# Kernel optimization log

Measured on AMD Instinct MI355X. Metric: run time of the kernel, lower is better.

Reference implementation:

```python
import jax, jax.numpy as jnp
import numpy as np

N = 50000
E = 800000
D = 128
NCLASS = 10


def setup_inputs() -> dict:
    key = jax.random.key(0)
    ks = jax.random.split(key, 12)
    stdv = 1.0 / np.sqrt(D)
    inp = {
        "x": jax.random.normal(ks[0], (N, D), dtype=jnp.float32),
        "edge_src": jax.random.randint(ks[1], (E,), 0, N, dtype=jnp.int32),
        "edge_dst": jax.random.randint(ks[2], (E,), 0, N, dtype=jnp.int32),
        "edge_weight": jax.random.uniform(ks[3], (E,), dtype=jnp.float32),
        "W1": jax.random.uniform(ks[4], (D, D), jnp.float32, -stdv, stdv),
        "b1": jax.random.uniform(ks[5], (D,), jnp.float32, -stdv, stdv),
        "W2": jax.random.uniform(ks[6], (D, D), jnp.float32, -stdv, stdv),
        "b2": jax.random.uniform(ks[7], (D,), jnp.float32, -stdv, stdv),
        "W3": jax.random.uniform(ks[8], (D, D), jnp.float32, -stdv, stdv),
        "b3": jax.random.uniform(ks[9], (D,), jnp.float32, -stdv, stdv),
        "lin_W": jax.random.normal(ks[10], (NCLASS, 3 * D), dtype=jnp.float32) * 0.05,
        "lin_b": jax.random.normal(ks[11], (NCLASS,), dtype=jnp.float32) * 0.05,
    }
    return inp


def _gcn_layer(h, W, b, edge_src, edge_dst, edge_weight):
    # support = h @ W  (dense GEMM), then spmm(adj, support) as gather-scale-scatter
    support = h @ W                                   # [N, out]
    msgs = support[edge_src] * edge_weight[:, None]   # [E, out]
    agg = jax.ops.segment_sum(msgs, edge_dst, num_segments=h.shape[0])
    return agg + b


def reference(x, edge_src, edge_dst, edge_weight, W1, b1, W2, b2, W3, b3, lin_W, lin_b):
    x1 = jax.nn.relu(_gcn_layer(x, W1, b1, edge_src, edge_dst, edge_weight))
    o1 = jnp.max(x1, axis=0)
    x2 = jax.nn.relu(_gcn_layer(x1, W2, b2, edge_src, edge_dst, edge_weight))
    o2 = jnp.max(x2, axis=0)
    x3 = _gcn_layer(x2, W3, b3, edge_src, edge_dst, edge_weight)
    o3 = jnp.max(x3, axis=0)
    lin_in = jnp.concatenate([o1, o2, o3], axis=0)    # [3*D]
    logits = lin_W @ lin_in + lin_b                   # [nclass]
    return jax.nn.log_softmax(logits, axis=0)
```

## Files before the change

kernel.cpp:

```cpp
#include <hip/hip_runtime.h>
#include <hip/hip_bf16.h>
#include <math.h>

#define NN 50000
#define NPAD 50048
#define NE 800000
#define DD 128
#define NCLS 10
#define SCAN_BLOCK 1024
#define NTILES ((NN + 1 + SCAN_BLOCK - 1) / SCAN_BLOCK)

typedef short s16x8 __attribute__((ext_vector_type(8)));
typedef float f32x4 __attribute__((ext_vector_type(4)));

__device__ __forceinline__ unsigned short f2bf(float x) {
  __hip_bfloat16 h = __float2bfloat16(x);
  return __builtin_bit_cast(unsigned short, h);
}
__device__ __forceinline__ float bflo(unsigned int u) { return __uint_as_float(u << 16); }
__device__ __forceinline__ float bfhi(unsigned int u) { return __uint_as_float(u & 0xFFFF0000u); }

__device__ __forceinline__ unsigned int fkey(float f) {
  unsigned int u = __float_as_uint(f);
  return u ^ ((u & 0x80000000u) ? 0xFFFFFFFFu : 0x80000000u);
}
__device__ __forceinline__ float funkey(unsigned int k) {
  unsigned int u = (k & 0x80000000u) ? (k ^ 0x80000000u) : ~k;
  return __uint_as_float(u);
}

__global__ void k_init(int* __restrict__ offs, unsigned int* __restrict__ omax) {
  int i = blockIdx.x * blockDim.x + threadIdx.x;
  if (i < NN + 1) offs[i] = 0;
  if (i < 3 * DD) omax[i] = 0u;
}

__global__ void k_count(const int* __restrict__ edst, int* __restrict__ offs) {
  int e = blockIdx.x * blockDim.x + threadIdx.x;
  if (e < NE) atomicAdd(&offs[edst[e] + 1], 1);
}

__global__ void k_scan_partial(const int* __restrict__ offs, int* __restrict__ bsum) {
  __shared__ int red[SCAN_BLOCK];
  int i = blockIdx.x * SCAN_BLOCK + threadIdx.x;
  red[threadIdx.x] = (i < NN + 1) ? offs[i] : 0;
  __syncthreads();
  for (int off = SCAN_BLOCK / 2; off > 0; off >>= 1) {
    if ((int)threadIdx.x < off) red[threadIdx.x] += red[threadIdx.x + off];
    __syncthreads();
  }
  if (threadIdx.x == 0) bsum[blockIdx.x] = red[0];
}

__global__ void k_scan_bsum(int* __restrict__ bsum) {
  if (threadIdx.x == 0) {
    int run = 0;
    for (int i = 0; i < NTILES; ++i) { int v = bsum[i]; bsum[i] = run; run += v; }
  }
}

__global__ void k_scan_final(int* __restrict__ offs, const int* __restrict__ bsum,
                             int* __restrict__ cursor) {
  __shared__ int tmp[SCAN_BLOCK];
  int i = blockIdx.x * SCAN_BLOCK + threadIdx.x;
  int v = (i < NN + 1) ? offs[i] : 0;
  tmp[threadIdx.x] = v;
  __syncthreads();
  for (int off = 1; off < SCAN_BLOCK; off <<= 1) {
    int t = ((int)threadIdx.x >= off) ? tmp[threadIdx.x - off] : 0;
    __syncthreads();
    tmp[threadIdx.x] += t;
    __syncthreads();
  }
  int incl = tmp[threadIdx.x] + bsum[blockIdx.x];
  if (i < NN + 1) {
    offs[i] = incl;
    if (i < NN) cursor[i] = incl;
  }
}

__global__ void k_fill(const int* __restrict__ esrc, const int* __restrict__ edst,
                       const float* __restrict__ ew, int* __restrict__ cursor,
                       int2* __restrict__ csr) {
  int e = blockIdx.x * blockDim.x + threadIdx.x;
  if (e < NE) {
    int d = edst[e];
    int p = atomicAdd(&cursor[d], 1);
    csr[p] = make_int2(esrc[e], __float_as_int(ew[e]));
  }
}

__global__ __launch_bounds__(256) void k_cvtW(const float* __restrict__ W1,
    const float* __restrict__ W2, const float* __restrict__ W3,
    unsigned short* __restrict__ WT1, unsigned short* __restrict__ WT2,
    unsigned short* __restrict__ WT3) {
  int i = blockIdx.x * 256 + threadIdx.x;
  if (i < DD * DD) {
    int k = i >> 7, c = i & 127;
    WT1[c * DD + k] = f2bf(W1[i]);
    WT2[c * DD + k] = f2bf(W2[i]);
    WT3[c * DD + k] = f2bf(W3[i]);
  }
}

template <int F32IN>
__global__ __launch_bounds__(256) void k_mm(const void* __restrict__ Hv,
                                            const unsigned short* __restrict__ Wt,
                                            unsigned short* __restrict__ S) {
  const int wave = threadIdx.x >> 6, lane = threadIdx.x & 63;
  const int gw = blockIdx.x * 4 + wave;
  const int r0 = (gw >> 1) * 32;
  const int cbase = (gw & 1) * 64;
  const int l15 = lane & 15, lk = (lane >> 4) * 8;

  s16x8 Af[4][4];
#pragma unroll
  for (int m = 0; m < 4; ++m)
#pragma unroll
    for (int ks = 0; ks < 4; ++ks)
      Af[m][ks] = *(const s16x8*)&Wt[(cbase + m * 16 + l15) * DD + ks * 32 + lk];

  s16x8 Bf[2][4];
#pragma unroll
  for (int n = 0; n < 2; ++n) {
    const int r = r0 + n * 16 + l15;
    if (F32IN) {
      const float* H = (const float*)Hv;
#pragma unroll
      for (int ks = 0; ks < 4; ++ks) {
        float4 a = make_float4(0.f, 0.f, 0.f, 0.f), b = a;
        if (r < NN) {
          a = *(const float4*)&H[(size_t)r * DD + ks * 32 + lk];
          b = *(const float4*)&H[(size_t)r * DD + ks * 32 + lk + 4];
        }
        s16x8 f;
        f[0] = (short)f2bf(a.x); f[1] = (short)f2bf(a.y);
        f[2] = (short)f2bf(a.z); f[3] = (short)f2bf(a.w);
        f[4] = (short)f2bf(b.x); f[5] = (short)f2bf(b.y);
        f[6] = (short)f2bf(b.z); f[7] = (short)f2bf(b.w);
        Bf[n][ks] = f;
      }
    } else {
      const unsigned short* H = (const unsigned short*)Hv;
#pragma unroll
      for (int ks = 0; ks < 4; ++ks)
        Bf[n][ks] = *(const s16x8*)&H[(size_t)r * DD + ks * 32 + lk];
    }
  }

  f32x4 acc[4][2];
#pragma unroll
  for (int m = 0; m < 4; ++m)
#pragma unroll
    for (int n = 0; n < 2; ++n) acc[m][n] = (f32x4){0.f, 0.f, 0.f, 0.f};

#pragma unroll
  for (int ks = 0; ks < 4; ++ks)
#pragma unroll
    for (int m = 0; m < 4; ++m)
#pragma unroll
      for (int n = 0; n < 2; ++n)
        acc[m][n] = __builtin_amdgcn_mfma_f32_16x16x32_bf16(Af[m][ks], Bf[n][ks],
                                                            acc[m][n], 0, 0, 0);

  const int csub = 4 * (lane >> 4);
#pragma unroll
  for (int m = 0; m < 4; ++m)
#pragma unroll
    for (int n = 0; n < 2; ++n) {
      uint2 pv;
      pv.x = (uint)f2bf(acc[m][n][0]) | ((uint)f2bf(acc[m][n][1]) << 16);
      pv.y = (uint)f2bf(acc[m][n][2]) | ((uint)f2bf(acc[m][n][3]) << 16);
      *(uint2*)&S[(size_t)(r0 + n * 16 + l15) * DD + cbase + m * 16 + csub] = pv;
    }
}

__device__ __forceinline__ void fma8(float* acc, float w, uint4 u) {
  acc[0] = fmaf(w, bflo(u.x), acc[0]);
  acc[1] = fmaf(w, bfhi(u.x), acc[1]);
  acc[2] = fmaf(w, bflo(u.y), acc[2]);
  acc[3] = fmaf(w, bfhi(u.y), acc[3]);
  acc[4] = fmaf(w, bflo(u.z), acc[4]);
  acc[5] = fmaf(w, bfhi(u.z), acc[5]);
  acc[6] = fmaf(w, bflo(u.w), acc[6]);
  acc[7] = fmaf(w, bfhi(u.w), acc[7]);
}

__global__ __launch_bounds__(256) void k_agg(const unsigned short* __restrict__ S,
                                             const int2* __restrict__ csr,
                                             const int* __restrict__ offs,
                                             const float* __restrict__ bias,
                                             unsigned short* __restrict__ Xout,
                                             unsigned int* __restrict__ omax,
                                             int do_relu) {
  __shared__ unsigned int cmax[DD];
  for (int i = threadIdx.x; i < DD; i += 256) cmax[i] = 0u;
  __syncthreads();
  const int lane = threadIdx.x & 63;
  const int wave = threadIdx.x >> 6;
  const int q = lane >> 4;
  const int t = lane & 15;
  const int gwave = blockIdx.x * 4 + wave;
  const int nwaves = gridDim.x * 4;

  float bcol[8];
  {
    float4 b0 = *(const float4*)&bias[t * 8];
    float4 b1 = *(const float4*)&bias[t * 8 + 4];
    bcol[0] = b0.x; bcol[1] = b0.y; bcol[2] = b0.z; bcol[3] = b0.w;
    bcol[4] = b1.x; bcol[5] = b1.y; bcol[6] = b1.z; bcol[7] = b1.w;
  }
  float mx[8];
#pragma unroll
  for (int j = 0; j < 8; ++j) mx[j] = -INFINITY;

  for (int d = gwave; d < NN; d += nwaves) {
    const int e0 = offs[d], e1 = offs[d + 1];
    float acc[8] = {0.f, 0.f, 0.f, 0.f, 0.f, 0.f, 0.f, 0.f};
    int e = e0 + q;
    const int nfull = (e1 - e0) >> 4;
    for (int s = 0; s < nfull; ++s, e += 16) {
      int2 c0 = csr[e];
      int2 c1 = csr[e + 4];
      int2 c2 = csr[e + 8];
      int2 c3 = csr[e + 12];
      uint4 u0 = *(const uint4*)&S[(size_t)c0.x * DD + t * 8];
      uint4 u1 = *(const uint4*)&S[(size_t)c1.x * DD + t * 8];
      uint4 u2 = *(const uint4*)&S[(size_t)c2.x * DD + t * 8];
      uint4 u3 = *(const uint4*)&S[(size_t)c3.x * DD + t * 8];
      fma8(acc, __int_as_float(c0.y), u0);
      fma8(acc, __int_as_float(c1.y), u1);
      fma8(acc, __int_as_float(c2.y), u2);
      fma8(acc, __int_as_float(c3.y), u3);
    }
    while (__any(e < e1)) {
      if (e < e1) {
        int2 c = csr[e];
        uint4 u = *(const uint4*)&S[(size_t)c.x * DD + t * 8];
        fma8(acc, __int_as_float(c.y), u);
      }
      e += 4;
    }
#pragma unroll
    for (int j = 0; j < 8; ++j) {
      acc[j] += __shfl_xor(acc[j], 16, 64);
      acc[j] += __shfl_xor(acc[j], 32, 64);
      acc[j] += bcol[j];
      if (do_relu) acc[j] = fmaxf(acc[j], 0.f);
      mx[j] = fmaxf(mx[j], acc[j]);
    }
    if (Xout && q == 0) {
      uint4 xv;
      xv.x = (uint)f2bf(acc[0]) | ((uint)f2bf(acc[1]) << 16);
      xv.y = (uint)f2bf(acc[2]) | ((uint)f2bf(acc[3]) << 16);
      xv.z = (uint)f2bf(acc[4]) | ((uint)f2bf(acc[5]) << 16);
      xv.w = (uint)f2bf(acc[6]) | ((uint)f2bf(acc[7]) << 16);
      *(uint4*)&Xout[(size_t)d * DD + t * 8] = xv;
    }
  }
  if (q == 0) {
#pragma unroll
    for (int j = 0; j < 8; ++j) atomicMax(&cmax[t * 8 + j], fkey(mx[j]));
  }
  __syncthreads();
  for (int i = threadIdx.x; i < DD; i += 256) atomicMax(&omax[i], cmax[i]);
}

__global__ void k_head(const unsigned int* __restrict__ omax,
                       const float* __restrict__ linW,
                       const float* __restrict__ linb,
                       float* __restrict__ out) {
  __shared__ float o[3 * DD];
  __shared__ float logits[NCLS];
  int t = threadIdx.x;
  if (t < 3 * DD) o[t] = funkey(omax[t]);
  __syncthreads();
  if (t < NCLS) {
    float acc = linb[t];
    for (int j = 0; j < 3 * DD; ++j) acc = fmaf(linW[t * 3 * DD + j], o[j], acc);
    logits[t] = acc;
  }
  __syncthreads();
  if (t == 0) {
    float m = -INFINITY;
    for (int c = 0; c < NCLS; ++c) m = fmaxf(m, logits[c]);
    float s = 0.f;
    for (int c = 0; c < NCLS; ++c) s += expf(logits[c] - m);
    float ls = logf(s);
    for (int c = 0; c < NCLS; ++c) out[c] = logits[c] - m - ls;
  }
}

extern "C" void kernel_launch(void* const* d_in, const int* in_sizes, int n_in,
                              void* d_out, int out_size, void* d_ws, size_t ws_size,
                              hipStream_t stream) {
  const float* x    = (const float*)d_in[0];
  const int*   esrc = (const int*)d_in[1];
  const int*   edst = (const int*)d_in[2];
  const float* ew   = (const float*)d_in[3];
  const float* W1   = (const float*)d_in[4];
  const float* b1   = (const float*)d_in[5];
  const float* W2   = (const float*)d_in[6];
  const float* b2   = (const float*)d_in[7];
  const float* W3   = (const float*)d_in[8];
  const float* b3   = (const float*)d_in[9];
  const float* linW = (const float*)d_in[10];
  const float* linb = (const float*)d_in[11];
  float* out = (float*)d_out;

  size_t off = 0;
  auto alloc = [&](size_t bytes) {
    void* p = (char*)d_ws + off;
    off += (bytes + 255) & ~(size_t)255;
    return p;
  };
  unsigned short* X1   = (unsigned short*)alloc((size_t)NPAD * DD * 2);
  unsigned short* X2   = (unsigned short*)alloc((size_t)NPAD * DD * 2);
  unsigned short* S    = (unsigned short*)alloc((size_t)NPAD * DD * 2);
  unsigned short* WT1  = (unsigned short*)alloc((size_t)DD * DD * 2);
  unsigned short* WT2  = (unsigned short*)alloc((size_t)DD * DD * 2);
  unsigned short* WT3  = (unsigned short*)alloc((size_t)DD * DD * 2);
  int*          offs   = (int*)alloc((NN + 1) * 4);
  int*          cursor = (int*)alloc(NN * 4);
  int2*         csr    = (int2*)alloc((size_t)NE * 8);
  unsigned int* omax   = (unsigned int*)alloc(3 * DD * 4);
  int*          bsum   = (int*)alloc(NTILES * 4);
  (void)ws_size; (void)n_in; (void)in_sizes; (void)out_size;

  k_init<<<(NN + 256) / 256, 256, 0, stream>>>(offs, omax);
  k_count<<<(NE + 255) / 256, 256, 0, stream>>>(edst, offs);
  k_scan_partial<<<NTILES, SCAN_BLOCK, 0, stream>>>(offs, bsum);
  k_scan_bsum<<<1, 64, 0, stream>>>(bsum);
  k_scan_final<<<NTILES, SCAN_BLOCK, 0, stream>>>(offs, bsum, cursor);
  k_fill<<<(NE + 255) / 256, 256, 0, stream>>>(esrc, edst, ew, cursor, csr);

  k_cvtW<<<(DD * DD + 255) / 256, 256, 0, stream>>>(W1, W2, W3, WT1, WT2, WT3);

  const int mm_grid = (NPAD / 32) * 2 / 4;
  k_mm<1><<<mm_grid, 256, 0, stream>>>(x, WT1, S);
  k_agg<<<2048, 256, 0, stream>>>(S, csr, offs, b1, X1, omax, 1);
  k_mm<0><<<mm_grid, 256, 0, stream>>>(X1, WT2, S);
  k_agg<<<2048, 256, 0, stream>>>(S, csr, offs, b2, X2, omax + DD, 1);
  k_mm<0><<<mm_grid, 256, 0, stream>>>(X2, WT3, S);
  k_agg<<<2048, 256, 0, stream>>>(S, csr, offs, b3, nullptr, omax + 2 * DD, 0);

  k_head<<<1, 384, 0, stream>>>(omax, linW, linb, out);
}
```

Baseline: 438.6 us.

## Stage GEMM row tiles in swizzled LDS and deepen aggregation gather unroll

The dense GEMM kernel now loads each 32-row input tile once into XOR-swizzled shared memory with coalesced 16-byte loads. Four waves each compute 32 output columns from that shared tile, and the result is staged back through LDS so the store to S is fully coalesced. Before, each wave loaded its own strided fragments straight from global memory. Separately, the aggregation loop is unrolled to 8 gathers in flight per lane, with a 16-edge remainder step, to expose more memory-level parallelism. The change adds barriers and LDS use per block, and the extra registers could reduce occupancy.

```diff
diff --git a/kernel.cpp b/kernel.cpp
--- a/kernel.cpp
+++ b/kernel.cpp
@@ -107,72 +107,97 @@
 __global__ __launch_bounds__(256) void k_mm(const void* __restrict__ Hv,
                                             const unsigned short* __restrict__ Wt,
                                             unsigned short* __restrict__ S) {
+  __shared__ unsigned short Hl[32 * DD];
+  char* lb = (char*)Hl;
   const int wave = threadIdx.x >> 6, lane = threadIdx.x & 63;
-  const int gw = blockIdx.x * 4 + wave;
-  const int r0 = (gw >> 1) * 32;
-  const int cbase = (gw & 1) * 64;
-  const int l15 = lane & 15, lk = (lane >> 4) * 8;
-
-  s16x8 Af[4][4];
-#pragma unroll
-  for (int m = 0; m < 4; ++m)
-#pragma unroll
-    for (int ks = 0; ks < 4; ++ks)
-      Af[m][ks] = *(const s16x8*)&Wt[(cbase + m * 16 + l15) * DD + ks * 32 + lk];
-
-  s16x8 Bf[2][4];
-#pragma unroll
-  for (int n = 0; n < 2; ++n) {
-    const int r = r0 + n * 16 + l15;
+  const int l15 = lane & 15, lk16 = (lane >> 4);
+  const int r0 = blockIdx.x * 32;
+
+#pragma unroll
+  for (int j = 0; j < 2; ++j) {
+    const int idx = threadIdx.x + j * 256;
+    const int B = idx * 16;
+    const int row = B >> 8;
+    const int addr = B ^ ((row & 7) << 4);
     if (F32IN) {
       const float* H = (const float*)Hv;
-#pragma unroll
-      for (int ks = 0; ks < 4; ++ks) {
-        float4 a = make_float4(0.f, 0.f, 0.f, 0.f), b = a;
-        if (r < NN) {
-          a = *(const float4*)&H[(size_t)r * DD + ks * 32 + lk];
-          b = *(const float4*)&H[(size_t)r * DD + ks * 32 + lk + 4];
-        }
-        s16x8 f;
-        f[0] = (short)f2bf(a.x); f[1] = (short)f2bf(a.y);
-        f[2] = (short)f2bf(a.z); f[3] = (short)f2bf(a.w);
-        f[4] = (short)f2bf(b.x); f[5] = (short)f2bf(b.y);
-        f[6] = (short)f2bf(b.z); f[7] = (short)f2bf(b.w);
-        Bf[n][ks] = f;
+      const int r = r0 + row;
+      float4 a = make_float4(0.f, 0.f, 0.f, 0.f), b = a;
+      if (r < NN) {
+        const float* src = H + (size_t)r * DD + ((B & 255) >> 1);
+        a = *(const float4*)src;
+        b = *(const float4*)(src + 4);
       }
+      uint4 pv;
+      pv.x = (uint)f2bf(a.x) | ((uint)f2bf(a.y) << 16);
+      pv.y = (uint)f2bf(a.z) | ((uint)f2bf(a.w) << 16);
+      pv.z = (uint)f2bf(b.x) | ((uint)f2bf(b.y) << 16);
+      pv.w = (uint)f2bf(b.z) | ((uint)f2bf(b.w) << 16);
+      *(uint4*)(lb + addr) = pv;
     } else {
-      const unsigned short* H = (const unsigned short*)Hv;
-#pragma unroll
-      for (int ks = 0; ks < 4; ++ks)
-        Bf[n][ks] = *(const s16x8*)&H[(size_t)r * DD + ks * 32 + lk];
-    }
-  }
-
-  f32x4 acc[4][2];
-#pragma unroll
-  for (int m = 0; m < 4; ++m)
+      const char* H = (const char*)Hv;
+      uint4 v = *(const uint4*)(H + (size_t)r0 * 256 + B);
+      *(uint4*)(lb + addr) = v;
+    }
+  }
+  __syncthreads();
+
+  const int cbase = wave * 32;
+  s16x8 Af[2][4];
+#pragma unroll
+  for (int m = 0; m < 2; ++m)
+#pragma unroll
+    for (int ks = 0; ks < 4; ++ks)
+      Af[m][ks] = *(const s16x8*)&Wt[(cbase + m * 16 + l15) * DD + ks * 32 + lk16 * 8];
+
+  s16x8 Bf[2][4];
+#pragma unroll
+  for (int n = 0; n < 2; ++n) {
+    const int row = n * 16 + l15;
+#pragma unroll
+    for (int ks = 0; ks < 4; ++ks) {
+      const int B = row * 256 + ks * 64 + lk16 * 16;
+      Bf[n][ks] = *(const s16x8*)(lb + (B ^ ((row & 7) << 4)));
+    }
+  }
+
+  f32x4 acc[2][2];
+#pragma unroll
+  for (int m = 0; m < 2; ++m)
 #pragma unroll
     for (int n = 0; n < 2; ++n) acc[m][n] = (f32x4){0.f, 0.f, 0.f, 0.f};
 
 #pragma unroll
   for (int ks = 0; ks < 4; ++ks)
 #pragma unroll
-    for (int m = 0; m < 4; ++m)
+    for (int m = 0; m < 2; ++m)
 #pragma unroll
       for (int n = 0; n < 2; ++n)
         acc[m][n] = __builtin_amdgcn_mfma_f32_16x16x32_bf16(Af[m][ks], Bf[n][ks],
                                                             acc[m][n], 0, 0, 0);
 
-  const int csub = 4 * (lane >> 4);
-#pragma unroll
-  for (int m = 0; m < 4; ++m)
+  __syncthreads();
+#pragma unroll
+  for (int m = 0; m < 2; ++m)
 #pragma unroll
     for (int n = 0; n < 2; ++n) {
+      const int row = n * 16 + l15;
+      const int colb = (cbase + m * 16 + 4 * lk16) * 2;
+      const int B = row * 256 + colb;
       uint2 pv;
       pv.x = (uint)f2bf(acc[m][n][0]) | ((uint)f2bf(acc[m][n][1]) << 16);
       pv.y = (uint)f2bf(acc[m][n][2]) | ((uint)f2bf(acc[m][n][3]) << 16);
-      *(uint2*)&S[(size_t)(r0 + n * 16 + l15) * DD + cbase + m * 16 + csub] = pv;
-    }
+      *(uint2*)(lb + (B ^ ((row & 7) << 4))) = pv;
+    }
+  __syncthreads();
+#pragma unroll
+  for (int j = 0; j < 2; ++j) {
+    const int idx = threadIdx.x + j * 256;
+    const int B = idx * 16;
+    const int row = B >> 8;
+    uint4 v = *(const uint4*)(lb + (B ^ ((row & 7) << 4)));
+    *(uint4*)((char*)S + (size_t)r0 * 256 + B) = v;
+  }
 }
 
 __device__ __forceinline__ void fma8(float* acc, float w, uint4 u) {
@@ -202,6 +227,7 @@
   const int t = lane & 15;
   const int gwave = blockIdx.x * 4 + wave;
   const int nwaves = gridDim.x * 4;
+  const unsigned short* Scol = S + t * 8;
 
   float bcol[8];
   {
@@ -216,27 +242,49 @@
 
   for (int d = gwave; d < NN; d += nwaves) {
     const int e0 = offs[d], e1 = offs[d + 1];
+    const int nedge = e1 - e0;
     float acc[8] = {0.f, 0.f, 0.f, 0.f, 0.f, 0.f, 0.f, 0.f};
     int e = e0 + q;
-    const int nfull = (e1 - e0) >> 4;
-    for (int s = 0; s < nfull; ++s, e += 16) {
-      int2 c0 = csr[e];
-      int2 c1 = csr[e + 4];
-      int2 c2 = csr[e + 8];
-      int2 c3 = csr[e + 12];
-      uint4 u0 = *(const uint4*)&S[(size_t)c0.x * DD + t * 8];
-      uint4 u1 = *(const uint4*)&S[(size_t)c1.x * DD + t * 8];
-      uint4 u2 = *(const uint4*)&S[(size_t)c2.x * DD + t * 8];
-      uint4 u3 = *(const uint4*)&S[(size_t)c3.x * DD + t * 8];
-      fma8(acc, __int_as_float(c0.y), u0);
-      fma8(acc, __int_as_float(c1.y), u1);
-      fma8(acc, __int_as_float(c2.y), u2);
-      fma8(acc, __int_as_float(c3.y), u3);
+    int done = 0;
+    for (; done + 32 <= nedge; done += 32, e += 32) {
+      int2 a0 = csr[e];      int2 a1 = csr[e + 4];
+      int2 a2 = csr[e + 8];  int2 a3 = csr[e + 12];
+      int2 a4 = csr[e + 16]; int2 a5 = csr[e + 20];
+      int2 a6 = csr[e + 24]; int2 a7 = csr[e + 28];
+      uint4 u0 = *(const uint4*)&Scol[(size_t)a0.x * DD];
+      uint4 u1 = *(const uint4*)&Scol[(size_t)a1.x * DD];
+      uint4 u2 = *(const uint4*)&Scol[(size_t)a2.x * DD];
+      uint4 u3 = *(const uint4*)&Scol[(size_t)a3.x * DD];
+      uint4 u4 = *(const uint4*)&Scol[(size_t)a4.x * DD];
+      uint4 u5 = *(const uint4*)&Scol[(size_t)a5.x * DD];
+      uint4 u6 = *(const uint4*)&Scol[(size_t)a6.x * DD];
+      uint4 u7 = *(const uint4*)&Scol[(size_t)a7.x * DD];
+      fma8(acc, __int_as_float(a0.y), u0);
+      fma8(acc, __int_as_float(a1.y), u1);
+      fma8(acc, __int_as_float(a2.y), u2);
+      fma8(acc, __int_as_float(a3.y), u3);
+      fma8(acc, __int_as_float(a4.y), u4);
+      fma8(acc, __int_as_float(a5.y), u5);
+      fma8(acc, __int_as_float(a6.y), u6);
+      fma8(acc, __int_as_float(a7.y), u7);
+    }
+    if (done + 16 <= nedge) {
+      int2 a0 = csr[e];      int2 a1 = csr[e + 4];
+      int2 a2 = csr[e + 8];  int2 a3 = csr[e + 12];
+      uint4 u0 = *(const uint4*)&Scol[(size_t)a0.x * DD];
+      uint4 u1 = *(const uint4*)&Scol[(size_t)a1.x * DD];
+      uint4 u2 = *(const uint4*)&Scol[(size_t)a2.x * DD];
+      uint4 u3 = *(const uint4*)&Scol[(size_t)a3.x * DD];
+      fma8(acc, __int_as_float(a0.y), u0);
+      fma8(acc, __int_as_float(a1.y), u1);
+      fma8(acc, __int_as_float(a2.y), u2);
+      fma8(acc, __int_as_float(a3.y), u3);
+      done += 16; e += 16;
     }
     while (__any(e < e1)) {
       if (e < e1) {
         int2 c = csr[e];
-        uint4 u = *(const uint4*)&S[(size_t)c.x * DD + t * 8];
+        uint4 u = *(const uint4*)&Scol[(size_t)c.x * DD];
         fma8(acc, __int_as_float(c.y), u);
       }
       e += 4;
@@ -336,7 +384,7 @@
 
   k_cvtW<<<(DD * DD + 255) / 256, 256, 0, stream>>>(W1, W2, W3, WT1, WT2, WT3);
 
-  const int mm_grid = (NPAD / 32) * 2 / 4;
+  const int mm_grid = NPAD / 32;
   k_mm<1><<<mm_grid, 256, 0, stream>>>(x, WT1, S);
   k_agg<<<2048, 256, 0, stream>>>(S, csr, offs, b1, X1, omax, 1);
   k_mm<0><<<mm_grid, 256, 0, stream>>>(X1, WT2, S);
```

Result: faster. 429.1 us (-2.2%).
